# Kernel optimization log

Measured on AMD Instinct MI355X. Metric: run time of the kernel, lower is better.

The kernel has to match this reference:

```python
import jax, jax.numpy as jnp
import numpy as np

SCALE = 1.153
DROP_P = 0.3


def setup_inputs() -> dict:
    key = jax.random.key(0)
    k1, k2 = jax.random.split(key)
    x1 = jax.random.normal(k1, (16, 2048, 128), dtype=jnp.float32)
    x2 = jax.random.normal(k2, (16, 2048, 128), dtype=jnp.float32)
    return {"x1": x1, "x2": x2}


def reference(x1, x2):
    # scores: [B, Nq, Nk]
    scores = jnp.einsum('bqd,bkd->bqk', x1, x2) * SCALE
    probs = jax.nn.softmax(scores, axis=-1)
    # dropout (training=True, p=0.3): inverted dropout scaling
    keep = 1.0 - DROP_P
    mask = jax.random.bernoulli(jax.random.key(42), keep, probs.shape)
    probs = jnp.where(mask, probs / keep, 0.0).astype(probs.dtype)
    # output: [B, Nq, D]
    return jnp.einsum('bqk,bkd->bqd', probs, x2)
```

## Files before the change

kernel.cpp:

```cpp
#include <hip/hip_runtime.h>
#include <cstdint>
#include <cstddef>

#define NQ 2048
#define NK 2048
#define DH 128
#define SCALEF 1.153f
#define SCALE2 (1.153f * 1.44269504088896340736f)
#define KEEPF  0.7f

typedef _Float16 half8 __attribute__((ext_vector_type(8)));
typedef float  floatx4 __attribute__((ext_vector_type(4)));

__device__ __align__(16) unsigned g_mask[1u << 21];
__device__ int g_mask_ready = 0;
__device__ __align__(16) _Float16 g_kimg[16 * 32 * 8192];
__device__ __align__(16) _Float16 g_vimg[16 * 32 * 8192];
__device__ __align__(16) _Float16 g_po16[512][128][128];
__device__             float    g_pm[512][128];
__device__             float    g_pl[512][128];

__device__ __forceinline__ unsigned rotl(unsigned x, int r) {
  return __builtin_amdgcn_alignbit(x, x, 32 - r);
}
__device__ __forceinline__ void tf_round(unsigned& x0, unsigned& x1, int r) {
  x0 += x1;
  x1 = rotl(x1, r);
  x1 ^= x0;
}
#define KEEP_THRESH 0xB3333400u

__device__ __forceinline__ unsigned tf_keep(unsigned i) {
  const unsigned ks1 = 42u, ks2 = 0x1BD11BDAu ^ 42u;
  unsigned x0 = 0u;
  unsigned x1 = i + ks1;
  tf_round(x0,x1,13); tf_round(x0,x1,15); tf_round(x0,x1,26); tf_round(x0,x1, 6);
  x0 += ks1;  x1 += ks2 + 1u;
  tf_round(x0,x1,17); tf_round(x0,x1,29); tf_round(x0,x1,16); tf_round(x0,x1,24);
  x0 += ks2;  x1 += 2u;
  tf_round(x0,x1,13); tf_round(x0,x1,15); tf_round(x0,x1,26); tf_round(x0,x1, 6);
     x1 += ks1 + 3u;
  tf_round(x0,x1,17); tf_round(x0,x1,29); tf_round(x0,x1,16); tf_round(x0,x1,24);
  x0 += ks1;  x1 += ks2 + 4u;
  tf_round(x0,x1,13); tf_round(x0,x1,15); tf_round(x0,x1,26); tf_round(x0,x1, 6);
  x0 += ks2;  x1 += 5u;
  return (unsigned)((x0 ^ x1) < KEEP_THRESH);
}

__global__ __launch_bounds__(256) void prep(const float* __restrict__ x2) {
  __shared__ __align__(16) _Float16 Tt[128 * 32];
  const int blk = blockIdx.x;
  const int tid = threadIdx.x;
  const int b   = blk >> 6;
  const int k0  = (blk & 63) * 32;
  const int kt  = (blk & 63) >> 1;
  const size_t ibase = ((size_t)(b * 32 + kt)) * 8192;

  const float4* src = (const float4*)(x2 + ((size_t)(b * NK + k0)) * DH);
  #pragma unroll
  for (int i = 0; i < 4; ++i) {
    int idx = tid + i * 256;
    int k  = idx >> 5;
    int dc = idx & 31;
    float4 v = src[idx];
    union { _Float16 h[4]; uint2 u; } H;
    H.h[0] = (_Float16)v.x; H.h[1] = (_Float16)v.y;
    H.h[2] = (_Float16)v.z; H.h[3] = (_Float16)v.w;
    int r  = (k0 + k) & 63;
    int c8 = dc >> 1;
    *(uint2*)&g_kimg[ibase + r * 128 + ((c8 ^ (r & 15)) << 3) + (dc & 1) * 4] = H.u;
    #pragma unroll
    for (int j = 0; j < 4; ++j) {
      int d = dc * 4 + j;
      Tt[d * 32 + ((((k >> 3) ^ (d >> 2)) & 3) << 3) + (k & 7)] = H.h[j];
    }
  }
  __syncthreads();
  #pragma unroll
  for (int i = 0; i < 2; ++i) {
    int idx = tid + i * 256;
    int d  = idx >> 2;
    int ch = idx & 3;
    uint4 vt = *(const uint4*)&Tt[d * 32 + (((ch ^ (d >> 2)) & 3) << 3)];
    int ch_g = ((blk & 1) << 2) + ch;
    *(uint4*)&g_vimg[ibase + d * 64 + ((ch_g ^ (d & 7)) << 3)] = vt;
  }

  if (!g_mask_ready) {
    const unsigned g0 = (unsigned)blk * 256u + (unsigned)tid;
    #pragma unroll
    for (int t = 0; t < 8; ++t) {
      unsigned g    = g0 + (unsigned)t * 262144u;
      unsigned base = g << 5;
      unsigned word = 0u;
      #pragma unroll 4
      for (int j = 0; j < 32; ++j)
        word |= tf_keep(base + (unsigned)j) << j;
      g_mask[g] = word;
    }
  }
}

__global__ __launch_bounds__(256, 2) void attn_kernel(
    const float* __restrict__ x1)
{
  __shared__ __align__(16) _Float16 Ksh[64 * 128];
  __shared__ __align__(16) _Float16 Vt[128 * 64];
  __shared__ __align__(16) _Float16 Ps[128 * 72];

  const int tid = threadIdx.x;
  const int blk = blockIdx.x;
  const int b     = ((blk & 7) << 1) | ((blk >> 3) & 1);
  const int h     = (blk >> 4) & 1;
  const int qt    = blk >> 5;
  const int qbase = qt * 128;
  const int kv0   = h << 10;
  const int lane = tid & 63, w = tid >> 6;
  const int quad = lane >> 4, c16 = lane & 15;

  half8 qf[2][4];
  #pragma unroll
  for (int mi = 0; mi < 2; ++mi) {
    const float* qrow = x1 +
        ((size_t)(b * NQ + qbase + w * 32 + mi * 16 + c16)) * DH;
    #pragma unroll
    for (int c = 0; c < 4; ++c) {
      float4 v0 = *(const float4*)&qrow[c * 32 + quad * 8];
      float4 v1 = *(const float4*)&qrow[c * 32 + quad * 8 + 4];
      qf[mi][c][0] = (_Float16)v0.x; qf[mi][c][1] = (_Float16)v0.y;
      qf[mi][c][2] = (_Float16)v0.z; qf[mi][c][3] = (_Float16)v0.w;
      qf[mi][c][4] = (_Float16)v1.x; qf[mi][c][5] = (_Float16)v1.y;
      qf[mi][c][6] = (_Float16)v1.z; qf[mi][c][7] = (_Float16)v1.w;
    }
  }

  floatx4 acc[2][8];
  #pragma unroll
  for (int mi = 0; mi < 2; ++mi)
    #pragma unroll
    for (int i = 0; i < 8; ++i) acc[mi][i] = (floatx4){0.f, 0.f, 0.f, 0.f};
  float m_i[2][4], l_i[2][4];
  #pragma unroll
  for (int mi = 0; mi < 2; ++mi)
    #pragma unroll
    for (int r = 0; r < 4; ++r) { m_i[mi][r] = -INFINITY; l_i[mi][r] = 0.f; }

  const unsigned mrow0 = (unsigned)(b * NQ + qbase + w * 32 + quad * 4) * 64u;
  const unsigned mrow1 = mrow0 + 16u * 64u;

  for (int kv = 0; kv < 1024; kv += 64) {
    const int kvg = kv0 + kv;
    __syncthreads();

    {
      const size_t ib = ((size_t)(b * 32) + (size_t)(kvg >> 6)) * 8192;
      #pragma unroll
      for (int t = 0; t < 4; ++t) {
        int e = (tid + t * 256) * 8;
        *(uint4*)&Ksh[e] = *(const uint4*)&g_kimg[ib + e];
        *(uint4*)&Vt[e]  = *(const uint4*)&g_vimg[ib + e];
      }
    }
    __syncthreads();

    uint2 mwa0 = *(const uint2*)&g_mask[mrow0 +   0 + (unsigned)(kvg >> 5)];
    uint2 mwa1 = *(const uint2*)&g_mask[mrow0 +  64 + (unsigned)(kvg >> 5)];
    uint2 mwa2 = *(const uint2*)&g_mask[mrow0 + 128 + (unsigned)(kvg >> 5)];
    uint2 mwa3 = *(const uint2*)&g_mask[mrow0 + 192 + (unsigned)(kvg >> 5)];
    uint2 mwb0 = *(const uint2*)&g_mask[mrow1 +   0 + (unsigned)(kvg >> 5)];
    uint2 mwb1 = *(const uint2*)&g_mask[mrow1 +  64 + (unsigned)(kvg >> 5)];
    uint2 mwb2 = *(const uint2*)&g_mask[mrow1 + 128 + (unsigned)(kvg >> 5)];
    uint2 mwb3 = *(const uint2*)&g_mask[mrow1 + 192 + (unsigned)(kvg >> 5)];

    floatx4 S0[4], S1[4];
    #pragma unroll
    for (int nt = 0; nt < 4; ++nt) {
      S0[nt] = (floatx4){0.f, 0.f, 0.f, 0.f};
      S1[nt] = (floatx4){0.f, 0.f, 0.f, 0.f};
      int row = nt * 16 + c16;
      int rbase = row * 128, rx = row & 15;
      #pragma unroll
      for (int c = 0; c < 4; ++c) {
        int addr = rbase + (((c * 4 + quad) ^ rx) << 3);
        half8 kh = *(const half8*)&Ksh[addr];
        S0[nt] = __builtin_amdgcn_mfma_f32_16x16x32_f16(qf[0][c], kh, S0[nt], 0, 0, 0);
        S1[nt] = __builtin_amdgcn_mfma_f32_16x16x32_f16(qf[1][c], kh, S1[nt], 0, 0, 0);
      }
    }

    #pragma unroll
    for (int mi = 0; mi < 2; ++mi) {
      floatx4* S = (mi == 0) ? S0 : S1;
      #pragma unroll
      for (int nt = 0; nt < 4; ++nt)
        #pragma unroll
        for (int r = 0; r < 4; ++r) S[nt][r] *= SCALE2;

      float mx[4];
      #pragma unroll
      for (int r = 0; r < 4; ++r)
        mx[r] = fmaxf(fmaxf(S[0][r], S[1][r]), fmaxf(S[2][r], S[3][r]));
      #pragma unroll
      for (int off = 1; off < 16; off <<= 1)
        #pragma unroll
        for (int r = 0; r < 4; ++r)
          mx[r] = fmaxf(mx[r], __shfl_xor(mx[r], off));

      float alpha[4];
      #pragma unroll
      for (int r = 0; r < 4; ++r) {
        float mo = m_i[mi][r];
        float mn = fmaxf(mo, mx[r]);
        m_i[mi][r] = mn;
        alpha[r] = exp2f(mo - mn);
        l_i[mi][r] *= alpha[r];
      }
      float p[4][4];
      #pragma unroll
      for (int nt = 0; nt < 4; ++nt)
        #pragma unroll
        for (int r = 0; r < 4; ++r)
          p[nt][r] = exp2f(S[nt][r] - m_i[mi][r]);
      #pragma unroll
      for (int r = 0; r < 4; ++r)
        l_i[mi][r] += (p[0][r] + p[1][r]) + (p[2][r] + p[3][r]);
      #pragma unroll
      for (int dt = 0; dt < 8; ++dt)
        #pragma unroll
        for (int r = 0; r < 4; ++r) acc[mi][dt][r] *= alpha[r];

      unsigned long long mm[4];
      if (mi == 0) {
        mm[0] = (unsigned long long)mwa0.x | ((unsigned long long)mwa0.y << 32);
        mm[1] = (unsigned long long)mwa1.x | ((unsigned long long)mwa1.y << 32);
        mm[2] = (unsigned long long)mwa2.x | ((unsigned long long)mwa2.y << 32);
        mm[3] = (unsigned long long)mwa3.x | ((unsigned long long)mwa3.y << 32);
      } else {
        mm[0] = (unsigned long long)mwb0.x | ((unsigned long long)mwb0.y << 32);
        mm[1] = (unsigned long long)mwb1.x | ((unsigned long long)mwb1.y << 32);
        mm[2] = (unsigned long long)mwb2.x | ((unsigned long long)mwb2.y << 32);
        mm[3] = (unsigned long long)mwb3.x | ((unsigned long long)mwb3.y << 32);
      }
      #pragma unroll
      for (int r = 0; r < 4; ++r) {
        #pragma unroll
        for (int nt = 0; nt < 4; ++nt) {
          int bitpos = nt * 16 + c16;
          float pv = ((mm[r] >> bitpos) & 1ull) ? p[nt][r] : 0.0f;
          Ps[(w * 32 + mi * 16 + quad * 4 + r) * 72 + nt * 16 + c16] = (_Float16)pv;
        }
      }
    }

    #pragma unroll
    for (int kc = 0; kc < 2; ++kc) {
      half8 af0 = *(const half8*)&Ps[(w * 32 +      c16) * 72 + kc * 32 + quad * 8];
      half8 af1 = *(const half8*)&Ps[(w * 32 + 16 + c16) * 72 + kc * 32 + quad * 8];
      #pragma unroll
      for (int dt = 0; dt < 8; ++dt) {
        int d = dt * 16 + c16;
        half8 bf = *(const half8*)&Vt[d * 64 + ((((kc << 2) + quad) ^ (d & 7)) << 3)];
        acc[0][dt] = __builtin_amdgcn_mfma_f32_16x16x32_f16(af0, bf, acc[0][dt], 0, 0, 0);
        acc[1][dt] = __builtin_amdgcn_mfma_f32_16x16x32_f16(af1, bf, acc[1][dt], 0, 0, 0);
      }
    }
  }

  const int pidx = ((b * 16 + qt) << 1) + h;
  #pragma unroll
  for (int mi = 0; mi < 2; ++mi) {
    #pragma unroll
    for (int off = 1; off < 16; off <<= 1)
      #pragma unroll
      for (int r = 0; r < 4; ++r)
        l_i[mi][r] += __shfl_xor(l_i[mi][r], off);
    if (c16 == 0) {
      #pragma unroll
      for (int r = 0; r < 4; ++r) {
        int row = w * 32 + mi * 16 + quad * 4 + r;
        g_pm[pidx][row] = m_i[mi][r];
        g_pl[pidx][row] = l_i[mi][r];
      }
    }
    #pragma unroll
    for (int dt = 0; dt < 8; ++dt)
      #pragma unroll
      for (int r = 0; r < 4; ++r)
        g_po16[pidx][w * 32 + mi * 16 + quad * 4 + r][dt * 16 + c16] =
            (_Float16)acc[mi][dt][r];
  }
}

__global__ __launch_bounds__(256) void merge_out(float* __restrict__ out) {
  __shared__ float sa1[128], sa2[128], sinv[128];
  const int blk = blockIdx.x;
  const int tid = threadIdx.x;
  if (blk == 0 && tid == 0) g_mask_ready = 1;
  const int b  = blk >> 4;
  const int qt = blk & 15;
  const int p0 = ((b * 16 + qt) << 1);

  if (tid < 128) {
    float m1 = g_pm[p0][tid],     m2 = g_pm[p0 + 1][tid];
    float l1 = g_pl[p0][tid],     l2 = g_pl[p0 + 1][tid];
    float m  = fmaxf(m1, m2);
    float a1 = exp2f(m1 - m),     a2 = exp2f(m2 - m);
    sa1[tid] = a1; sa2[tid] = a2;
    sinv[tid] = 1.0f / (KEEPF * (l1 * a1 + l2 * a2));
  }
  __syncthreads();

  const uint2* p1 = (const uint2*)&g_po16[p0][0][0];
  const uint2* p2 = (const uint2*)&g_po16[p0 + 1][0][0];
  float4* dst = (float4*)(out + ((size_t)(b * NQ + qt * 128)) * DH);
  #pragma unroll
  for (int i = 0; i < 16; ++i) {
    int idx = tid + i * 256;
    int row = idx >> 5;
    uint2 u1 = p1[idx], u2 = p2[idx];
    const _Float16* h1 = (const _Float16*)&u1;
    const _Float16* h2 = (const _Float16*)&u2;
    float a1 = sa1[row], a2 = sa2[row], inv = sinv[row];
    float4 o;
    o.x = ((float)h1[0] * a1 + (float)h2[0] * a2) * inv;
    o.y = ((float)h1[1] * a1 + (float)h2[1] * a2) * inv;
    o.z = ((float)h1[2] * a1 + (float)h2[2] * a2) * inv;
    o.w = ((float)h1[3] * a1 + (float)h2[3] * a2) * inv;
    dst[idx] = o;
  }
}

extern "C" void kernel_launch(void* const* d_in, const int* in_sizes, int n_in,
                              void* d_out, int out_size, void* d_ws, size_t ws_size,
                              hipStream_t stream) {
  const float* x1 = (const float*)d_in[0];
  const float* x2 = (const float*)d_in[1];
  float* out = (float*)d_out;

  prep<<<1024, 256, 0, stream>>>(x2);
  attn_kernel<<<512, 256, 0, stream>>>(x1);
  merge_out<<<256, 256, 0, stream>>>(out);
}
```

Measured before the change: 156.9 us.

## Double-buffer K/V tiles with async global-to-LDS loads and swizzle P tile

K and V tiles are now loaded straight from global memory into LDS with global_load_lds, into two ping-pong buffers. The next 64-key tile is fetched while the current one is computed, so the separate synchronous copy phase inside the loop goes away. The P staging buffer also changes from a padded 72-stride layout to a 64-stride XOR-swizzled layout, to avoid LDS bank conflicts while using less memory. The trade-off is more LDS per block, which could limit occupancy. Correctness also depends on the barrier waiting for the async LDS writes to finish.

```diff
diff --git a/kernel.cpp b/kernel.cpp
--- a/kernel.cpp
+++ b/kernel.cpp
@@ -47,6 +47,12 @@
   return (unsigned)((x0 ^ x1) < KEEP_THRESH);
 }
 
+__device__ __forceinline__ void gll16(const _Float16* g, _Float16* l) {
+  __builtin_amdgcn_global_load_lds(
+      (const __attribute__((address_space(1))) unsigned int*)g,
+      (__attribute__((address_space(3))) unsigned int*)l, 16, 0, 0);
+}
+
 __global__ __launch_bounds__(256) void prep(const float* __restrict__ x2) {
   __shared__ __align__(16) _Float16 Tt[128 * 32];
   const int blk = blockIdx.x;
@@ -104,9 +110,11 @@
 __global__ __launch_bounds__(256, 2) void attn_kernel(
     const float* __restrict__ x1)
 {
-  __shared__ __align__(16) _Float16 Ksh[64 * 128];
-  __shared__ __align__(16) _Float16 Vt[128 * 64];
-  __shared__ __align__(16) _Float16 Ps[128 * 72];
+  __shared__ __align__(16) _Float16 KshA[64 * 128];
+  __shared__ __align__(16) _Float16 KshB[64 * 128];
+  __shared__ __align__(16) _Float16 VtA[128 * 64];
+  __shared__ __align__(16) _Float16 VtB[128 * 64];
+  __shared__ __align__(16) _Float16 Ps[128 * 64];
 
   const int tid = threadIdx.x;
   const int blk = blockIdx.x;
@@ -148,123 +156,140 @@
   const unsigned mrow0 = (unsigned)(b * NQ + qbase + w * 32 + quad * 4) * 64u;
   const unsigned mrow1 = mrow0 + 16u * 64u;
 
-  for (int kv = 0; kv < 1024; kv += 64) {
-    const int kvg = kv0 + kv;
+  const int e0 = tid * 8;
+  const size_t ibb = (size_t)(b * 32) * 8192;
+
+#define ISSUE(KS, VT, kvn) do {                                             \
+    const size_t ib_ = ibb + (size_t)((kvn) >> 6) * 8192;                   \
+    gll16(&g_kimg[ib_ + e0],        &KS[e0]);                               \
+    gll16(&g_kimg[ib_ + e0 + 2048], &KS[e0 + 2048]);                        \
+    gll16(&g_kimg[ib_ + e0 + 4096], &KS[e0 + 4096]);                        \
+    gll16(&g_kimg[ib_ + e0 + 6144], &KS[e0 + 6144]);                        \
+    gll16(&g_vimg[ib_ + e0],        &VT[e0]);                               \
+    gll16(&g_vimg[ib_ + e0 + 2048], &VT[e0 + 2048]);                        \
+    gll16(&g_vimg[ib_ + e0 + 4096], &VT[e0 + 4096]);                        \
+    gll16(&g_vimg[ib_ + e0 + 6144], &VT[e0 + 6144]);                        \
+  } while (0)
+
+#define COMPUTE(KS, VT, KVG) do {                                           \
+    const int kvg_ = (KVG);                                                 \
+    uint2 mwa0 = *(const uint2*)&g_mask[mrow0 +   0 + (unsigned)(kvg_ >> 5)];\
+    uint2 mwa1 = *(const uint2*)&g_mask[mrow0 +  64 + (unsigned)(kvg_ >> 5)];\
+    uint2 mwa2 = *(const uint2*)&g_mask[mrow0 + 128 + (unsigned)(kvg_ >> 5)];\
+    uint2 mwa3 = *(const uint2*)&g_mask[mrow0 + 192 + (unsigned)(kvg_ >> 5)];\
+    uint2 mwb0 = *(const uint2*)&g_mask[mrow1 +   0 + (unsigned)(kvg_ >> 5)];\
+    uint2 mwb1 = *(const uint2*)&g_mask[mrow1 +  64 + (unsigned)(kvg_ >> 5)];\
+    uint2 mwb2 = *(const uint2*)&g_mask[mrow1 + 128 + (unsigned)(kvg_ >> 5)];\
+    uint2 mwb3 = *(const uint2*)&g_mask[mrow1 + 192 + (unsigned)(kvg_ >> 5)];\
+    floatx4 S0[4], S1[4];                                                   \
+    _Pragma("unroll")                                                       \
+    for (int nt = 0; nt < 4; ++nt) {                                        \
+      S0[nt] = (floatx4){0.f, 0.f, 0.f, 0.f};                               \
+      S1[nt] = (floatx4){0.f, 0.f, 0.f, 0.f};                               \
+      int row = nt * 16 + c16;                                              \
+      int rbase = row * 128, rx = row & 15;                                 \
+      _Pragma("unroll")                                                     \
+      for (int c = 0; c < 4; ++c) {                                         \
+        int addr = rbase + (((c * 4 + quad) ^ rx) << 3);                    \
+        half8 kh = *(const half8*)&KS[addr];                                \
+        S0[nt] = __builtin_amdgcn_mfma_f32_16x16x32_f16(qf[0][c], kh, S0[nt], 0, 0, 0); \
+        S1[nt] = __builtin_amdgcn_mfma_f32_16x16x32_f16(qf[1][c], kh, S1[nt], 0, 0, 0); \
+      }                                                                     \
+    }                                                                       \
+    _Pragma("unroll")                                                       \
+    for (int mi = 0; mi < 2; ++mi) {                                        \
+      floatx4* S = (mi == 0) ? S0 : S1;                                     \
+      _Pragma("unroll")                                                     \
+      for (int nt = 0; nt < 4; ++nt)                                        \
+        _Pragma("unroll")                                                   \
+        for (int r = 0; r < 4; ++r) S[nt][r] *= SCALE2;                     \
+      float mx[4];                                                          \
+      _Pragma("unroll")                                                     \
+      for (int r = 0; r < 4; ++r)                                           \
+        mx[r] = fmaxf(fmaxf(S[0][r], S[1][r]), fmaxf(S[2][r], S[3][r]));    \
+      _Pragma("unroll")                                                     \
+      for (int off = 1; off < 16; off <<= 1)                                \
+        _Pragma("unroll")                                                   \
+        for (int r = 0; r < 4; ++r)                                         \
+          mx[r] = fmaxf(mx[r], __shfl_xor(mx[r], off));                     \
+      float alpha[4];                                                       \
+      _Pragma("unroll")                                                     \
+      for (int r = 0; r < 4; ++r) {                                         \
+        float mo = m_i[mi][r];                                              \
+        float mn = fmaxf(mo, mx[r]);                                        \
+        m_i[mi][r] = mn;                                                    \
+        alpha[r] = exp2f(mo - mn);                                          \
+        l_i[mi][r] *= alpha[r];                                             \
+      }                                                                     \
+      float p[4][4];                                                        \
+      _Pragma("unroll")                                                     \
+      for (int nt = 0; nt < 4; ++nt)                                        \
+        _Pragma("unroll")                                                   \
+        for (int r = 0; r < 4; ++r)                                         \
+          p[nt][r] = exp2f(S[nt][r] - m_i[mi][r]);                          \
+      _Pragma("unroll")                                                     \
+      for (int r = 0; r < 4; ++r)                                           \
+        l_i[mi][r] += (p[0][r] + p[1][r]) + (p[2][r] + p[3][r]);            \
+      _Pragma("unroll")                                                     \
+      for (int dt = 0; dt < 8; ++dt)                                        \
+        _Pragma("unroll")                                                   \
+        for (int r = 0; r < 4; ++r) acc[mi][dt][r] *= alpha[r];             \
+      unsigned long long mm[4];                                             \
+      if (mi == 0) {                                                        \
+        mm[0] = (unsigned long long)mwa0.x | ((unsigned long long)mwa0.y << 32); \
+        mm[1] = (unsigned long long)mwa1.x | ((unsigned long long)mwa1.y << 32); \
+        mm[2] = (unsigned long long)mwa2.x | ((unsigned long long)mwa2.y << 32); \
+        mm[3] = (unsigned long long)mwa3.x | ((unsigned long long)mwa3.y << 32); \
+      } else {                                                              \
+        mm[0] = (unsigned long long)mwb0.x | ((unsigned long long)mwb0.y << 32); \
+        mm[1] = (unsigned long long)mwb1.x | ((unsigned long long)mwb1.y << 32); \
+        mm[2] = (unsigned long long)mwb2.x | ((unsigned long long)mwb2.y << 32); \
+        mm[3] = (unsigned long long)mwb3.x | ((unsigned long long)mwb3.y << 32); \
+      }                                                                     \
+      _Pragma("unroll")                                                     \
+      for (int r = 0; r < 4; ++r) {                                         \
+        int row = w * 32 + mi * 16 + quad * 4 + r;                          \
+        _Pragma("unroll")                                                   \
+        for (int nt = 0; nt < 4; ++nt) {                                    \
+          int bitpos = nt * 16 + c16;                                       \
+          float pv = ((mm[r] >> bitpos) & 1ull) ? p[nt][r] : 0.0f;          \
+          Ps[row * 64 + (((nt * 2 + (c16 >> 3)) ^ (row & 7)) << 3) + (c16 & 7)] = (_Float16)pv; \
+        }                                                                   \
+      }                                                                     \
+    }                                                                       \
+                                  \
+    {                                                                       \
+      int row0 = w * 32 + c16, row1 = row0 + 16;                            \
+      _Pragma("unroll")                                                     \
+      for (int kc = 0; kc < 2; ++kc) {                                      \
+        half8 af0 = *(const half8*)&Ps[row0 * 64 + (((kc * 4 + quad) ^ (row0 & 7)) << 3)]; \
+        half8 af1 = *(const half8*)&Ps[row1 * 64 + (((kc * 4 + quad) ^ (row1 & 7)) << 3)]; \
+        _Pragma("unroll")                                                   \
+        for (int dt = 0; dt < 8; ++dt) {                                    \
+          int d = dt * 16 + c16;                                            \
+          half8 bf = *(const half8*)&VT[d * 64 + ((((kc << 2) + quad) ^ (d & 7)) << 3)]; \
+          acc[0][dt] = __builtin_amdgcn_mfma_f32_16x16x32_f16(af0, bf, acc[0][dt], 0, 0, 0); \
+          acc[1][dt] = __builtin_amdgcn_mfma_f32_16x16x32_f16(af1, bf, acc[1][dt], 0, 0, 0); \
+        }                                                                   \
+      }                                                                     \
+    }                                                                       \
+  } while (0)
+
+  ISSUE(KshA, VtA, kv0);
+
+  for (int kv = 0; kv < 1024; kv += 128) {
+    const int kvgA = kv0 + kv;
+    const int kvgB = kvgA + 64;
     __syncthreads();
-
-    {
-      const size_t ib = ((size_t)(b * 32) + (size_t)(kvg >> 6)) * 8192;
-      #pragma unroll
-      for (int t = 0; t < 4; ++t) {
-        int e = (tid + t * 256) * 8;
-        *(uint4*)&Ksh[e] = *(const uint4*)&g_kimg[ib + e];
-        *(uint4*)&Vt[e]  = *(const uint4*)&g_vimg[ib + e];
-      }
-    }
+    ISSUE(KshB, VtB, kvgB);
+    COMPUTE(KshA, VtA, kvgA);
     __syncthreads();
-
-    uint2 mwa0 = *(const uint2*)&g_mask[mrow0 +   0 + (unsigned)(kvg >> 5)];
-    uint2 mwa1 = *(const uint2*)&g_mask[mrow0 +  64 + (unsigned)(kvg >> 5)];
-    uint2 mwa2 = *(const uint2*)&g_mask[mrow0 + 128 + (unsigned)(kvg >> 5)];
-    uint2 mwa3 = *(const uint2*)&g_mask[mrow0 + 192 + (unsigned)(kvg >> 5)];
-    uint2 mwb0 = *(const uint2*)&g_mask[mrow1 +   0 + (unsigned)(kvg >> 5)];
-    uint2 mwb1 = *(const uint2*)&g_mask[mrow1 +  64 + (unsigned)(kvg >> 5)];
-    uint2 mwb2 = *(const uint2*)&g_mask[mrow1 + 128 + (unsigned)(kvg >> 5)];
-    uint2 mwb3 = *(const uint2*)&g_mask[mrow1 + 192 + (unsigned)(kvg >> 5)];
-
-    floatx4 S0[4], S1[4];
-    #pragma unroll
-    for (int nt = 0; nt < 4; ++nt) {
-      S0[nt] = (floatx4){0.f, 0.f, 0.f, 0.f};
-      S1[nt] = (floatx4){0.f, 0.f, 0.f, 0.f};
-      int row = nt * 16 + c16;
-      int rbase = row * 128, rx = row & 15;
-      #pragma unroll
-      for (int c = 0; c < 4; ++c) {
-        int addr = rbase + (((c * 4 + quad) ^ rx) << 3);
-        half8 kh = *(const half8*)&Ksh[addr];
-        S0[nt] = __builtin_amdgcn_mfma_f32_16x16x32_f16(qf[0][c], kh, S0[nt], 0, 0, 0);
-        S1[nt] = __builtin_amdgcn_mfma_f32_16x16x32_f16(qf[1][c], kh, S1[nt], 0, 0, 0);
-      }
-    }
-
-    #pragma unroll
-    for (int mi = 0; mi < 2; ++mi) {
-      floatx4* S = (mi == 0) ? S0 : S1;
-      #pragma unroll
-      for (int nt = 0; nt < 4; ++nt)
-        #pragma unroll
-        for (int r = 0; r < 4; ++r) S[nt][r] *= SCALE2;
-
-      float mx[4];
-      #pragma unroll
-      for (int r = 0; r < 4; ++r)
-        mx[r] = fmaxf(fmaxf(S[0][r], S[1][r]), fmaxf(S[2][r], S[3][r]));
-      #pragma unroll
-      for (int off = 1; off < 16; off <<= 1)
-        #pragma unroll
-        for (int r = 0; r < 4; ++r)
-          mx[r] = fmaxf(mx[r], __shfl_xor(mx[r], off));
-
-      float alpha[4];
-      #pragma unroll
-      for (int r = 0; r < 4; ++r) {
-        float mo = m_i[mi][r];
-        float mn = fmaxf(mo, mx[r]);
-        m_i[mi][r] = mn;
-        alpha[r] = exp2f(mo - mn);
-        l_i[mi][r] *= alpha[r];
-      }
-      float p[4][4];
-      #pragma unroll
-      for (int nt = 0; nt < 4; ++nt)
-        #pragma unroll
-        for (int r = 0; r < 4; ++r)
-          p[nt][r] = exp2f(S[nt][r] - m_i[mi][r]);
-      #pragma unroll
-      for (int r = 0; r < 4; ++r)
-        l_i[mi][r] += (p[0][r] + p[1][r]) + (p[2][r] + p[3][r]);
-      #pragma unroll
-      for (int dt = 0; dt < 8; ++dt)
-        #pragma unroll
-        for (int r = 0; r < 4; ++r) acc[mi][dt][r] *= alpha[r];
-
-      unsigned long long mm[4];
-      if (mi == 0) {
-        mm[0] = (unsigned long long)mwa0.x | ((unsigned long long)mwa0.y << 32);
-        mm[1] = (unsigned long long)mwa1.x | ((unsigned long long)mwa1.y << 32);
-        mm[2] = (unsigned long long)mwa2.x | ((unsigned long long)mwa2.y << 32);
-        mm[3] = (unsigned long long)mwa3.x | ((unsigned long long)mwa3.y << 32);
-      } else {
-        mm[0] = (unsigned long long)mwb0.x | ((unsigned long long)mwb0.y << 32);
-        mm[1] = (unsigned long long)mwb1.x | ((unsigned long long)mwb1.y << 32);
-        mm[2] = (unsigned long long)mwb2.x | ((unsigned long long)mwb2.y << 32);
-        mm[3] = (unsigned long long)mwb3.x | ((unsigned long long)mwb3.y << 32);
-      }
-      #pragma unroll
-      for (int r = 0; r < 4; ++r) {
-        #pragma unroll
-        for (int nt = 0; nt < 4; ++nt) {
-          int bitpos = nt * 16 + c16;
-          float pv = ((mm[r] >> bitpos) & 1ull) ? p[nt][r] : 0.0f;
-          Ps[(w * 32 + mi * 16 + quad * 4 + r) * 72 + nt * 16 + c16] = (_Float16)pv;
-        }
-      }
-    }
-
-    #pragma unroll
-    for (int kc = 0; kc < 2; ++kc) {
-      half8 af0 = *(const half8*)&Ps[(w * 32 +      c16) * 72 + kc * 32 + quad * 8];
-      half8 af1 = *(const half8*)&Ps[(w * 32 + 16 + c16) * 72 + kc * 32 + quad * 8];
-      #pragma unroll
-      for (int dt = 0; dt < 8; ++dt) {
-        int d = dt * 16 + c16;
-        half8 bf = *(const half8*)&Vt[d * 64 + ((((kc << 2) + quad) ^ (d & 7)) << 3)];
-        acc[0][dt] = __builtin_amdgcn_mfma_f32_16x16x32_f16(af0, bf, acc[0][dt], 0, 0, 0);
-        acc[1][dt] = __builtin_amdgcn_mfma_f32_16x16x32_f16(af1, bf, acc[1][dt], 0, 0, 0);
-      }
-    }
-  }
+    if (kv + 128 < 1024)
+      ISSUE(KshA, VtA, kvgA + 128);
+    COMPUTE(KshB, VtB, kvgB);
+  }
+#undef ISSUE
+#undef COMPUTE
 
   const int pidx = ((b * 16 + qt) << 1) + h;
   #pragma unroll
```

After: 229.5 us. 46.3% more time.
